# Kernel tuning notes

Hardware: AMD Instinct MI355X
Metric: run time of the kernel (lower is better)

Reference implementation:

```python
import jax, jax.numpy as jnp
import numpy as np

B, N, SU, H, NC, NUM_ITER = 1024, 32, 8, 64, 4, 5
E = N * (N - 1)


def _edge_idx(n):
    # Fully-connected graph without self loops; edges grouped contiguously by
    # destination node so that blocks of (n-1) messages sum into one node
    # (matches the original Python segment-sum loop with step = n-1).
    idx = np.arange(n)
    temp_a = np.concatenate([np.delete(idx, j) for j in range(n)])  # sources
    temp_b = np.repeat(idx, n - 1)                                   # destinations
    return temp_a, temp_b


def _lin(x, W, b):
    return x @ W.T + b


def setup_inputs():
    key = jax.random.key(0)
    ks = jax.random.split(key, 20)
    f = jax.random.normal
    return {
        "read_gru": f(ks[0], (B, N, SU), jnp.float32),
        "gru_init": f(ks[1], (B, N, H), jnp.float32),
        "init_features": f(ks[2], (B, N, 3), jnp.float32),
        "edge_weight": f(ks[3], (B, E), jnp.float32),
        "noise_info": jax.random.uniform(ks[4], (B, 1), jnp.float32),
        "x_hat_EP": f(ks[5], (B, N), jnp.float32),
        "variance_EP": jax.random.uniform(ks[6], (B, N), jnp.float32),
        "W1a": f(ks[7], (SU, 3)) * 0.3, "b1a": jnp.zeros((SU,)),
        "W2a": f(ks[8], (H, 2 * SU + 2)) * 0.1, "b2a": jnp.zeros((H,)),
        "W2b": f(ks[9], (H // 2, H)) * 0.1, "b2b": jnp.zeros((H // 2,)),
        "W2c": f(ks[10], (SU, H // 2)) * 0.1, "b2c": jnp.zeros((SU,)),
        "Wih": f(ks[11], (3 * H, SU + 2)) * 0.1, "bih": jnp.zeros((3 * H,)),
        "Whh": f(ks[12], (3 * H, H)) * 0.1, "bhh": jnp.zeros((3 * H,)),
        "W3a": f(ks[13], (H, SU)) * 0.1, "b3a": jnp.zeros((H,)),
        "W3b": f(ks[14], (H // 2, H)) * 0.1, "b3b": jnp.zeros((H // 2,)),
        "W3c": f(ks[15], (NC, H // 2)) * 0.1, "b3c": jnp.zeros((NC,)),
        "W4": f(ks[16], (SU, H)) * 0.1, "b4": jnp.zeros((SU,)),
        "GNN_iter": 0,
    }


def reference(read_gru, gru_init, init_features, edge_weight, noise_info,
              x_hat_EP, variance_EP,
              W1a, b1a, W2a, b2a, W2b, b2b, W2c, b2c,
              Wih, bih, Whh, bhh,
              W3a, b3a, W3b, b3b, W3c, b3c, W4, b4, GNN_iter):
    b, n = init_features.shape[0], init_features.shape[1]
    temp_a, temp_b = _edge_idx(n)
    e = temp_a.shape[0]
    edge_e = edge_weight[:, :, None]                              # [B,E,1]
    noise_e = jnp.broadcast_to(noise_info, (b, e))[:, :, None]    # [B,E,1]
    gru_hidden = gru_init
    for it in range(NUM_ITER):
        if it == 0 and GNN_iter == 0:
            init_nodes = _lin(init_features, W1a, b1a)            # [B,N,SU]
        else:
            init_nodes = read_gru
        s1 = init_nodes[:, temp_a, :]                             # gather sources
        s2 = init_nodes[:, temp_b, :]                             # gather dests
        comb = jnp.concatenate([s1, s2, edge_e, noise_e], axis=2) # [B,E,2SU+2]
        m = jax.nn.relu(_lin(comb, W2a, b2a))
        m = jax.nn.relu(_lin(m, W2b, b2b))
        m = jax.nn.relu(_lin(m, W2c, b2c))                        # [B,E,SU]
        # contiguous blocks of (n-1) messages per destination node
        sum_msgs = m.reshape(b, n, n - 1, -1).sum(axis=2)         # [B,N,SU]
        gin = jnp.concatenate(
            [sum_msgs, x_hat_EP[:, :, None], variance_EP[:, :, None]], axis=2)
        # GRUCell applied per node
        gi = _lin(gin, Wih, bih)
        gh = _lin(gru_hidden, Whh, bhh)
        i_r, i_z, i_n = jnp.split(gi, 3, axis=-1)
        h_r, h_z, h_n = jnp.split(gh, 3, axis=-1)
        r = jax.nn.sigmoid(i_r + h_r)
        z = jax.nn.sigmoid(i_z + h_z)
        cand = jnp.tanh(i_n + r * h_n)
        gru_hidden = (1.0 - z) * cand + z * gru_hidden
        read_gru = _lin(gru_hidden, W4, b4)
    # readout (no activations in original forward)
    p_y_x = _lin(_lin(_lin(read_gru, W3a, b3a), W3b, b3b), W3c, b3c)
    return (p_y_x, read_gru, gru_hidden)
```

## Files before the change

kernel.cpp:

```cpp
#include <hip/hip_runtime.h>
#include <hip/hip_bf16.h>

#define BB 1024
#define NN 32
#define SUD 8
#define HD 64
#define NCD 4
#define ED 992
#define NITER 5

#define O_W2AT 0
#define O_B2A  1152
#define O_W2B  1216
#define O_B2B  3264
#define O_W2CT 3296
#define O_B2C  3552
#define O_WIHT 3560
#define O_BIH  5480
#define O_WHHT 5672
#define O_BHH  17960
#define O_W4T  18152
#define O_B4   18664
#define O_W3AT 18672
#define O_B3A  19184
#define O_W3BT 19248
#define O_B3B  21296
#define O_W3CT 21328
#define O_B3C  21456
#define O_W1AT 21460
#define O_B1A  21484
#define W_TOTAL 21492
#define O_WIHP 21492
#define W_TOTAL2 25332

#define FRAG_B2   0
#define FRAG_C    2048
#define FRAG_WHH  2560
#define FRAG_A2P  14848
#define FRAG_TOTAL 18944
#define PREP_TOTAL (W_TOTAL2 + FRAG_TOTAL)

typedef const float* fwp;
typedef __attribute__((ext_vector_type(8))) short short8;
typedef __attribute__((ext_vector_type(4))) float float4v;
typedef __attribute__((ext_vector_type(2))) float float2v;

__device__ __forceinline__ short bf16r(float x) {
  __hip_bfloat16 h = __float2bfloat16(x);
  return __builtin_bit_cast(short, h);
}

__global__ void prep_weights(fwp W2a, fwp b2a, fwp W2b, fwp b2b, fwp W2c, fwp b2c,
                             fwp Wih, fwp bih, fwp Whh, fwp bhh,
                             fwp W3a, fwp b3a, fwp W3b, fwp b3b, fwp W3c, fwp b3c,
                             fwp W4, fwp b4, fwp W1a, fwp b1a, float* __restrict__ ws) {
  int idx = blockIdx.x * 256 + threadIdx.x;
  if (idx >= PREP_TOTAL) return;
  if (idx >= W_TOTAL2) {
    __hip_bfloat16* wbw = (__hip_bfloat16*)(ws + W_TOTAL2);
    int e = idx - W_TOTAL2;
    float v;
    if (e < 2048) {
      int j = e & 7, L = (e >> 3) & 63, hs = e >> 9;
      int h = hs >> 1, s = hs & 1;
      v = W2b[(2 * (L & 15) + h) * 64 + s * 32 + ((L >> 4) & 3) * 8 + j];
    } else if (e < 2560) {
      int e2 = e - 2048;
      int j = e2 & 7, L = (e2 >> 3) & 63;
      int su = L & 15, q = L >> 4;
      v = (su < 8) ? W2c[su * 32 + q * 8 + j] : 0.f;
    } else if (e < 14848) {
      int e2 = e - 2560;
      int j = e2 & 7, L = (e2 >> 3) & 63, nts = e2 >> 9;
      int nt = nts >> 1, s = nts & 1;
      v = Whh[(nt * 16 + (L & 15)) * 64 + s * 32 + ((L >> 4) & 3) * 8 + j];
    } else {
      int e2 = e - 14848;
      int j = e2 & 7, L = (e2 >> 3) & 63, nt = e2 >> 9;
      int col = L & 15, kq = L >> 4;
      v = 0.f;
      if (kq == 0) v = (nt < 4) ? W2a[(nt * 16 + col) * 18 + j]
                                : W2a[((nt - 4) * 16 + col) * 18 + 8 + j];
    }
    wbw[e] = __float2bfloat16(v);
    return;
  }
  if (idx >= W_TOTAL) {
    int p = idx - O_WIHP;
    int o = p / 20, k = (p % 20) >> 1;
    ws[idx] = Wih[o * 10 + k];
    return;
  }
  float v;
  if (idx < O_B2A)       { int p = idx;          int su = p / 64, f = p % 64;   v = W2a[f * 18 + su]; }
  else if (idx < O_W2B)  { v = b2a[idx - O_B2A]; }
  else if (idx < O_B2B)  { v = W2b[idx - O_W2B]; }
  else if (idx < O_W2CT) { v = b2b[idx - O_B2B]; }
  else if (idx < O_B2C)  { int p = idx - O_W2CT; int o = p / 8, su = p % 8;     v = W2c[su * 32 + o]; }
  else if (idx < O_WIHT) { v = b2c[idx - O_B2C]; }
  else if (idx < O_BIH)  { int p = idx - O_WIHT; int k = p / 192, o = p % 192;  v = Wih[o * 10 + k]; }
  else if (idx < O_WHHT) { v = bih[idx - O_BIH]; }
  else if (idx < O_BHH)  {
    int p = idx - O_WHHT;
    if (p < 3072) {
      unsigned packed = 0;
#pragma unroll
      for (int h = 0; h < 2; ++h) {
        int e = 2 * p + h;
        int j = e & 7, L = (e >> 3) & 63, nt = e >> 9;
        int k = ((L >> 4) & 3) * 8 + j;
        float vv = (k < 10) ? Wih[(nt * 16 + (L & 15)) * 10 + k] : 0.f;
        unsigned us = (unsigned short)bf16r(vv);
        packed |= us << (16 * h);
      }
      ws[idx] = __builtin_bit_cast(float, packed);
      return;
    }
    int k = p / 192, o = p % 192;  v = Whh[o * 64 + k];
  }
  else if (idx < O_W4T)  { v = bhh[idx - O_BHH]; }
  else if (idx < O_B4)   { int p = idx - O_W4T;  int k = p / 8, su = p % 8;     v = W4[su * 64 + k]; }
  else if (idx < O_W3AT) { v = b4[idx - O_B4]; }
  else if (idx < O_B3A)  { int p = idx - O_W3AT; int k = p / 64, f = p % 64;    v = W3a[f * 8 + k]; }
  else if (idx < O_W3BT) { v = b3a[idx - O_B3A]; }
  else if (idx < O_B3B)  { int p = idx - O_W3BT; int k = p / 32, f = p % 32;    v = W3b[f * 64 + k]; }
  else if (idx < O_W3CT) { v = b3b[idx - O_B3B]; }
  else if (idx < O_B3C)  { int p = idx - O_W3CT; int k = p / 4, c = p % 4;      v = W3c[c * 32 + k]; }
  else if (idx < O_W1AT) { v = b3c[idx - O_B3C]; }
  else if (idx < O_B1A)  { int p = idx - O_W1AT; int c = p / 8, su = p % 8;     v = W1a[su * 3 + c]; }
  else                   { v = b1a[idx - O_B1A]; }
  ws[idx] = v;
}

#define DO_STEP2(AROW, EWV, KOFF, Y0, Y1, W0, W1, FH0, FH1, ACC0, ACC1)        \
  {                                                                            \
    float4v x0 = *(const float4v*)&sA1[(AROW) * 68 + (KOFF)];                  \
    float4v x1 = *(const float4v*)&sA1[(AROW) * 68 + (KOFF) + 4];              \
    float4v z4 = {0.f, 0.f, 0.f, 0.f};                                         \
    float4v t0 = (x0 + Y0) + (EWV) * W0;                                       \
    float4v t1 = (x1 + Y1) + (EWV) * W1;                                       \
    t0 = __builtin_elementwise_max(t0, z4);                                    \
    t1 = __builtin_elementwise_max(t1, z4);                                    \
    short8 ahi;                                                                \
    ahi[0] = bf16r(t0.x); ahi[1] = bf16r(t0.y); ahi[2] = bf16r(t0.z);          \
    ahi[3] = bf16r(t0.w); ahi[4] = bf16r(t1.x); ahi[5] = bf16r(t1.y);          \
    ahi[6] = bf16r(t1.z); ahi[7] = bf16r(t1.w);                                \
    ACC0 = __builtin_amdgcn_mfma_f32_16x16x32_bf16(ahi, FH0, ACC0, 0, 0, 0);   \
    ACC1 = __builtin_amdgcn_mfma_f32_16x16x32_bf16(ahi, FH1, ACC1, 0, 0, 0);   \
  }

#define LAUNDER(v) __asm__ __volatile__("" : "+v"(v))

__global__ __launch_bounds__(256, 4) void gnn_fused(
    const float* __restrict__ read_gru_in,
    const float* __restrict__ gru_init,
    const float* __restrict__ feat,
    const float* __restrict__ edge_w,
    const float* __restrict__ noise_in,
    const float* __restrict__ xhat,
    const float* __restrict__ vep,
    const int* __restrict__ gnn_iter_p,
    const float* __restrict__ ws,
    const float* __restrict__ W4g,
    float* __restrict__ out)
{
  __shared__ __attribute__((aligned(16))) char spool[23040];
  __shared__ __attribute__((aligned(16))) float sH[NN * 68];
  __shared__ float sNodes[NN * 9];
  __shared__ float sSum[NN * 8];
  __shared__ float sEw[ED];
  __shared__ float sC1[64];
  __shared__ float sWew[64];
  __shared__ float sX[NN];
  __shared__ float sV[NN];

  float* const sA1 = (float*)spool;
  float* const sA2 = (float*)(spool + 8704);
  __hip_bfloat16* const sM2 = (__hip_bfloat16*)(spool + 17408);

  const int b = blockIdx.x;
  const int t = threadIdx.x;
  const int lane = t & 63;
  const int wv = t >> 6;
  const int quad = lane >> 4;
  const int lm = lane & 15;

  const __hip_bfloat16* wb = (const __hip_bfloat16*)(ws + W_TOTAL2);

  float noi = noise_in[b];
  for (int e = t; e < ED; e += 256) sEw[e] = edge_w[b * ED + e];
  if (t < NN) { sX[t] = xhat[b * NN + t]; sV[t] = vep[b * NN + t]; }
  if (t < 64) {
    sC1[t]  = ws[O_B2A + t] + noi * ws[O_W2AT + 17 * 64 + t];
    sWew[t] = ws[O_W2AT + 16 * 64 + t];
  }
#pragma unroll
  for (int i = 0; i < 8; ++i) {
    int p = t + 256 * i;
    sH[(p >> 6) * 68 + (p & 63)] = gru_init[b * (NN * HD) + p];
  }
  {
    const int git = gnn_iter_p[0];
    int n = t >> 3, su = t & 7;
    float acc;
    if (git == 0) {
      acc = ws[O_B1A + su];
#pragma unroll
      for (int c = 0; c < 3; ++c)
        acc += ws[O_W1AT + c * 8 + su] * feat[b * (NN * 3) + n * 3 + c];
    } else {
      acc = read_gru_in[b * (NN * SUD) + t];
    }
    sNodes[n * 9 + su] = acc;
  }
  __syncthreads();

  for (int it = 0; it < NITER; ++it) {
    int ive = 0; LAUNDER(ive);
    const float* wsle = ws + ive;
    const __hip_bfloat16* wble = wb + ive;
    short8 fbh00 = *(const short8*)(wble + FRAG_B2 + (0 * 64 + lane) * 8);
    short8 fbh01 = *(const short8*)(wble + FRAG_B2 + (1 * 64 + lane) * 8);
    short8 fbh10 = *(const short8*)(wble + FRAG_B2 + (2 * 64 + lane) * 8);
    short8 fbh11 = *(const short8*)(wble + FRAG_B2 + (3 * 64 + lane) * 8);
    short8 fcf   = *(const short8*)(wble + FRAG_C + lane * 8);
    const float2v b2bv = *(const float2v*)&wsle[O_B2B + 2 * lm];
    const float   b2cl = wsle[O_B2C + lm];

    {
      int iva = 0; LAUNDER(iva);
      const __hip_bfloat16* fp = wb + FRAG_A2P + iva;
      short8 aN[2];
#pragma unroll
      for (int mt = 0; mt < 2; ++mt) {
        short8 a = {0, 0, 0, 0, 0, 0, 0, 0};
        if (quad == 0) {
          const float* np = &sNodes[(mt * 16 + lm) * 9];
#pragma unroll
          for (int q = 0; q < 8; ++q) a[q] = bf16r(np[q]);
        }
        aN[mt] = a;
      }
      const int f = wv * 16 + lm;
      const float c1f = sC1[f];
#pragma unroll
      for (int half = 0; half < 2; ++half) {
        short8 bfr = *(const short8*)(fp + ((half * 4 + wv) * 64 + lane) * 8);
#pragma unroll
        for (int mt = 0; mt < 2; ++mt) {
          float4v acc = {0.f, 0.f, 0.f, 0.f};
          acc = __builtin_amdgcn_mfma_f32_16x16x32_bf16(aN[mt], bfr, acc, 0, 0, 0);
#pragma unroll
          for (int r = 0; r < 4; ++r) {
            int node = mt * 16 + quad * 4 + r;
            if (half == 0) sA1[node * 68 + f] = acc[r];
            else           sA2[node * 68 + f] = acc[r] + c1f;
          }
        }
      }
    }
    __syncthreads();

    {
      int ivz = 0; LAUNDER(ivz);
      __hip_bfloat16* m2w = sM2 + wv * (16 * 44);
      const int kq0 = quad * 8, kq1 = 32 + quad * 8;
      float4v wwA = *(const float4v*)&sWew[ivz + kq0];
      float4v wwB = *(const float4v*)&sWew[ivz + kq0 + 4];
      float4v wwC = *(const float4v*)&sWew[ivz + kq1];
      float4v wwD = *(const float4v*)&sWew[ivz + kq1 + 4];
      const float4v binit0 = {b2bv.x, b2bv.x, b2bv.x, b2bv.x};
      const float4v binit1 = {b2bv.y, b2bv.y, b2bv.y, b2bv.y};
      const float4v cinit  = {b2cl, b2cl, b2cl, b2cl};
      const int kkB = 16 + lm;
      const int kkB2 = (kkB < 31) ? kkB : 0;
      for (int ni = 0; ni < 8; ++ni) {
        const int jj = wv * 8 + ni;
        const int a0 = lm + (lm >= jj ? 1 : 0);
        const int a1 = kkB2 + (kkB2 >= jj ? 1 : 0);
        const float ew0 = sEw[ivz + jj * 31 + lm];
        const float ew1 = (kkB < 31) ? sEw[ivz + jj * 31 + kkB] : 0.f;
        float4v yA = *(const float4v*)&sA2[jj * 68 + kq0];
        float4v yB = *(const float4v*)&sA2[jj * 68 + kq0 + 4];
        float4v yC = *(const float4v*)&sA2[jj * 68 + kq1];
        float4v yD = *(const float4v*)&sA2[jj * 68 + kq1 + 4];
        float4v acc00 = binit0;
        float4v acc01 = binit1;
        DO_STEP2(a0, ew0, kq0, yA, yB, wwA, wwB, fbh00, fbh10, acc00, acc01);
        DO_STEP2(a0, ew0, kq1, yC, yD, wwC, wwD, fbh01, fbh11, acc00, acc01);
#pragma unroll
        for (int r = 0; r < 4; ++r) {
          float m20 = fmaxf(acc00[r], 0.f);
          float m21 = fmaxf(acc01[r], 0.f);
          ushort2 pp;
          pp.x = (unsigned short)bf16r(m20);
          pp.y = (unsigned short)bf16r(m21);
          *(ushort2*)(m2w + (quad * 4 + r) * 44 + 2 * lm) = pp;
        }
        float4v acc10 = binit0;
        float4v acc11 = binit1;
        DO_STEP2(a1, ew1, kq0, yA, yB, wwA, wwB, fbh00, fbh10, acc10, acc11);
        DO_STEP2(a1, ew1, kq1, yC, yD, wwC, wwD, fbh01, fbh11, acc10, acc11);
        __asm__ __volatile__("" ::: "memory");
        float psum;
        {
          short8 ac = *(const short8*)(m2w + lm * 44 + quad * 8);
          float4v c3 = cinit;
          c3 = __builtin_amdgcn_mfma_f32_16x16x32_bf16(ac, fcf, c3, 0, 0, 0);
          psum  = fmaxf(c3[0], 0.f);
          psum += fmaxf(c3[1], 0.f);
          psum += fmaxf(c3[2], 0.f);
          psum += fmaxf(c3[3], 0.f);
        }
        __asm__ __volatile__("" ::: "memory");
#pragma unroll
        for (int r = 0; r < 4; ++r) {
          float m20 = fmaxf(acc10[r], 0.f);
          float m21 = fmaxf(acc11[r], 0.f);
          ushort2 pp;
          pp.x = (unsigned short)bf16r(m20);
          pp.y = (unsigned short)bf16r(m21);
          *(ushort2*)(m2w + (quad * 4 + r) * 44 + 2 * lm) = pp;
        }
        __asm__ __volatile__("" ::: "memory");
        {
          short8 ac = *(const short8*)(m2w + lm * 44 + quad * 8);
          float4v c3 = cinit;
          c3 = __builtin_amdgcn_mfma_f32_16x16x32_bf16(ac, fcf, c3, 0, 0, 0);
#pragma unroll
          for (int r = 0; r < 4; ++r) {
            float v = fmaxf(c3[r], 0.f);
            if (r == 3) v = (quad == 3) ? 0.f : v;
            psum += v;
          }
        }
        __asm__ __volatile__("" ::: "memory");
        psum += __shfl_xor(psum, 16);
        psum += __shfl_xor(psum, 32);
        if (lane < 8) sSum[jj * 8 + lane] = psum;
      }
    }
    __syncthreads();

    {
      int ivg = 0; LAUNDER(ivg);
      const __hip_bfloat16* wbl = wb + ivg;
      const __hip_bfloat16* wihf = (const __hip_bfloat16*)(ws + O_WHHT) + ivg;
      short8 aH[2][2];
      short8 aG[2];
#pragma unroll
      for (int mt = 0; mt < 2; ++mt) {
#pragma unroll
        for (int s = 0; s < 2; ++s) {
          const float* hp = &sH[(mt * 16 + lm) * 68 + s * 32 + quad * 8];
          float4v h0 = *(const float4v*)hp;
          float4v h1 = *(const float4v*)(hp + 4);
          short8 a;
          a[0] = bf16r(h0.x); a[1] = bf16r(h0.y); a[2] = bf16r(h0.z); a[3] = bf16r(h0.w);
          a[4] = bf16r(h1.x); a[5] = bf16r(h1.y); a[6] = bf16r(h1.z); a[7] = bf16r(h1.w);
          aH[mt][s] = a;
        }
        short8 g = {0, 0, 0, 0, 0, 0, 0, 0};
        int nrow = mt * 16 + lm;
        if (quad == 0) {
          float4v s0 = *(const float4v*)&sSum[nrow * 8];
          float4v s1 = *(const float4v*)&sSum[nrow * 8 + 4];
          g[0] = bf16r(s0.x); g[1] = bf16r(s0.y); g[2] = bf16r(s0.z); g[3] = bf16r(s0.w);
          g[4] = bf16r(s1.x); g[5] = bf16r(s1.y); g[6] = bf16r(s1.z); g[7] = bf16r(s1.w);
        } else if (quad == 1) {
          g[0] = bf16r(sX[nrow]);
          g[1] = bf16r(sV[nrow]);
        }
        aG[mt] = g;
      }
      const float4v zz4 = {0.f, 0.f, 0.f, 0.f};
      float4v pr0, pr1, pz0, pz1, phn0, phn1, pin0, pin1;
      {
        int gnt = wv;
        short8 bh0 = *(const short8*)(wbl + FRAG_WHH + ((gnt * 2 + 0) * 64 + lane) * 8);
        short8 bh1 = *(const short8*)(wbl + FRAG_WHH + ((gnt * 2 + 1) * 64 + lane) * 8);
        short8 bwi = *(const short8*)(wihf + (gnt * 64 + lane) * 8);
        pr0 = __builtin_amdgcn_mfma_f32_16x16x32_bf16(aG[0], bwi, zz4, 0, 0, 0);
        pr0 = __builtin_amdgcn_mfma_f32_16x16x32_bf16(aH[0][0], bh0, pr0, 0, 0, 0);
        pr0 = __builtin_amdgcn_mfma_f32_16x16x32_bf16(aH[0][1], bh1, pr0, 0, 0, 0);
        pr1 = __builtin_amdgcn_mfma_f32_16x16x32_bf16(aG[1], bwi, zz4, 0, 0, 0);
        pr1 = __builtin_amdgcn_mfma_f32_16x16x32_bf16(aH[1][0], bh0, pr1, 0, 0, 0);
        pr1 = __builtin_amdgcn_mfma_f32_16x16x32_bf16(aH[1][1], bh1, pr1, 0, 0, 0);
      }
      {
        int gnt = 4 + wv;
        short8 bh0 = *(const short8*)(wbl + FRAG_WHH + ((gnt * 2 + 0) * 64 + lane) * 8);
        short8 bh1 = *(const short8*)(wbl + FRAG_WHH + ((gnt * 2 + 1) * 64 + lane) * 8);
        short8 bwi = *(const short8*)(wihf + (gnt * 64 + lane) * 8);
        pz0 = __builtin_amdgcn_mfma_f32_16x16x32_bf16(aG[0], bwi, zz4, 0, 0, 0);
        pz0 = __builtin_amdgcn_mfma_f32_16x16x32_bf16(aH[0][0], bh0, pz0, 0, 0, 0);
        pz0 = __builtin_amdgcn_mfma_f32_16x16x32_bf16(aH[0][1], bh1, pz0, 0, 0, 0);
        pz1 = __builtin_amdgcn_mfma_f32_16x16x32_bf16(aG[1], bwi, zz4, 0, 0, 0);
        pz1 = __builtin_amdgcn_mfma_f32_16x16x32_bf16(aH[1][0], bh0, pz1, 0, 0, 0);
        pz1 = __builtin_amdgcn_mfma_f32_16x16x32_bf16(aH[1][1], bh1, pz1, 0, 0, 0);
      }
      {
        int gnt = 8 + wv;
        short8 bh0 = *(const short8*)(wbl + FRAG_WHH + ((gnt * 2 + 0) * 64 + lane) * 8);
        short8 bh1 = *(const short8*)(wbl + FRAG_WHH + ((gnt * 2 + 1) * 64 + lane) * 8);
        short8 bwi = *(const short8*)(wihf + (gnt * 64 + lane) * 8);
        phn0 = __builtin_amdgcn_mfma_f32_16x16x32_bf16(aH[0][0], bh0, zz4, 0, 0, 0);
        phn0 = __builtin_amdgcn_mfma_f32_16x16x32_bf16(aH[0][1], bh1, phn0, 0, 0, 0);
        phn1 = __builtin_amdgcn_mfma_f32_16x16x32_bf16(aH[1][0], bh0, zz4, 0, 0, 0);
        phn1 = __builtin_amdgcn_mfma_f32_16x16x32_bf16(aH[1][1], bh1, phn1, 0, 0, 0);
        pin0 = __builtin_amdgcn_mfma_f32_16x16x32_bf16(aG[0], bwi, zz4, 0, 0, 0);
        pin1 = __builtin_amdgcn_mfma_f32_16x16x32_bf16(aG[1], bwi, zz4, 0, 0, 0);
      }
      const int c = wv * 16 + lm;
      const float br  = ws[O_BIH + c]       + ws[O_BHH + c];
      const float bz  = ws[O_BIH + 64 + c]  + ws[O_BHH + 64 + c];
      const float bni = ws[O_BIH + 128 + c];
      const float bnh = ws[O_BHH + 128 + c];
      float4v hn0, hn1;
#pragma unroll
      for (int mt = 0; mt < 2; ++mt) {
#pragma unroll
        for (int rr = 0; rr < 4; ++rr) {
          int n = mt * 16 + quad * 4 + rr;
          float pre_r = ((mt == 0) ? pr0[rr]  : pr1[rr])  + br;
          float pre_z = ((mt == 0) ? pz0[rr]  : pz1[rr])  + bz;
          float i_n   = ((mt == 0) ? pin0[rr] : pin1[rr]) + bni;
          float h_n   = ((mt == 0) ? phn0[rr] : phn1[rr]) + bnh;
          float er = __expf(-pre_r);
          float r = __builtin_amdgcn_rcpf(1.f + er);
          float ez = __expf(-pre_z);
          float z = __builtin_amdgcn_rcpf(1.f + ez);
          float cd = i_n + r * h_n;
          float e2 = __expf(2.f * cd);
          float th = 1.f - 2.f * __builtin_amdgcn_rcpf(e2 + 1.f);
          float hv = sH[n * 68 + c];
          float hnew = th + z * (hv - th);
          if (mt == 0) hn0[rr] = hnew; else hn1[rr] = hnew;
        }
      }
      __syncthreads();
#pragma unroll
      for (int rr = 0; rr < 4; ++rr) {
        sH[(quad * 4 + rr) * 68 + c]      = hn0[rr];
        sH[(16 + quad * 4 + rr) * 68 + c] = hn1[rr];
      }
    }
    __syncthreads();

    {
      int ivw = 0; LAUNDER(ivw);
      int n = t >> 3, su = t & 7;
      const float* w4r = W4g + ivw + su * 64;
      float4v acc4 = {0.f, 0.f, 0.f, 0.f};
#pragma unroll
      for (int k = 0; k < 64; k += 4) {
        float4v w = *(const float4v*)&w4r[k];
        float4v h = *(const float4v*)&sH[n * 68 + k];
        acc4 += w * h;
      }
      sNodes[n * 9 + su] = ws[O_B4 + su] + ((acc4.x + acc4.y) + (acc4.z + acc4.w));
    }
    __syncthreads();
  }

#pragma unroll
  for (int i = 0; i < 8; ++i) {
    int p = t + 256 * i;
    int n = p >> 6, f = p & 63;
    float acc = ws[O_B3A + f];
#pragma unroll
    for (int k = 0; k < 8; ++k) acc += ws[O_W3AT + k * 64 + f] * sNodes[n * 9 + k];
    sA1[n * 68 + f] = acc;
  }
  __syncthreads();
#pragma unroll
  for (int i = 0; i < 4; ++i) {
    int p = t + 256 * i;
    int n = p >> 5, f = p & 31;
    float c0 = 0.f, c1v = 0.f, c2 = 0.f, c3v = 0.f;
#pragma unroll
    for (int k = 0; k < 64; k += 4) {
      c0  += ws[O_W3BT + (k + 0) * 32 + f] * sA1[n * 68 + k + 0];
      c1v += ws[O_W3BT + (k + 1) * 32 + f] * sA1[n * 68 + k + 1];
      c2  += ws[O_W3BT + (k + 2) * 32 + f] * sA1[n * 68 + k + 2];
      c3v += ws[O_W3BT + (k + 3) * 32 + f] * sA1[n * 68 + k + 3];
    }
    sA2[n * 33 + f] = ws[O_B3B + f] + ((c0 + c1v) + (c2 + c3v));
  }
  __syncthreads();
  if (t < 128) {
    int n = t >> 2, c = t & 3;
    float acc = ws[O_B3C + c];
#pragma unroll
    for (int k = 0; k < 32; ++k) acc += ws[O_W3CT + k * 4 + c] * sA2[n * 33 + k];
    out[b * (NN * NCD) + t] = acc;
  }
  out[BB * NN * NCD + b * (NN * SUD) + t] = sNodes[(t >> 3) * 9 + (t & 7)];
#pragma unroll
  for (int i = 0; i < 8; ++i) {
    int p = t + 256 * i;
    out[BB * NN * NCD + BB * NN * SUD + b * (NN * HD) + p] =
        sH[(p >> 6) * 68 + (p & 63)];
  }
}

extern "C" void kernel_launch(void* const* d_in, const int* in_sizes, int n_in,
                              void* d_out, int out_size, void* d_ws, size_t ws_size,
                              hipStream_t stream) {
  typedef const float* F32;
  F32 read_gru = (F32)d_in[0];
  F32 gru_init = (F32)d_in[1];
  F32 feat     = (F32)d_in[2];
  F32 edge_w   = (F32)d_in[3];
  F32 noise    = (F32)d_in[4];
  F32 xh       = (F32)d_in[5];
  F32 vp       = (F32)d_in[6];
  F32 W1a = (F32)d_in[7];  F32 b1a = (F32)d_in[8];
  F32 W2a = (F32)d_in[9];  F32 b2a = (F32)d_in[10];
  F32 W2b = (F32)d_in[11]; F32 b2b = (F32)d_in[12];
  F32 W2c = (F32)d_in[13]; F32 b2c = (F32)d_in[14];
  F32 Wih = (F32)d_in[15]; F32 bih = (F32)d_in[16];
  F32 Whh = (F32)d_in[17]; F32 bhh = (F32)d_in[18];
  F32 W3a = (F32)d_in[19]; F32 b3a = (F32)d_in[20];
  F32 W3b = (F32)d_in[21]; F32 b3b = (F32)d_in[22];
  F32 W3c = (F32)d_in[23]; F32 b3c = (F32)d_in[24];
  F32 W4  = (F32)d_in[25]; F32 b4  = (F32)d_in[26];
  const int* git = (const int*)d_in[27];
  float* ws = (float*)d_ws;

  prep_weights<<<(PREP_TOTAL + 255) / 256, 256, 0, stream>>>(
      W2a, b2a, W2b, b2b, W2c, b2c, Wih, bih, Whh, bhh,
      W3a, b3a, W3b, b3b, W3c, b3c, W4, b4, W1a, b1a, ws);

  gnn_fused<<<BB, 256, 0, stream>>>(read_gru, gru_init, feat, edge_w, noise,
                                    xh, vp, git, ws, W4, (float*)d_out);
}
```

Baseline: 245.5 us.

## Fold W4 readout into first message layer weights for later iterations

Precomputes the products W2a·W4 (for both source and destination halves) and b4·W2a at weight-prep time, so iterations after the first compute the first message-layer pre-activations directly from the GRU hidden state with K=64 MFMAs. This removes the per-iteration W4 projection and its barrier, moving it to a single computation after the loop. In exchange it reuses the W2B/W2CT/WIHP workspace slots for the folded weights and runs four MFMAs per tile instead of one, and rounds the folded weights and hidden state to bf16.

```diff
diff --git a/kernel.cpp b/kernel.cpp
--- a/kernel.cpp
+++ b/kernel.cpp
@@ -87,16 +87,58 @@
   }
   if (idx >= W_TOTAL) {
     int p = idx - O_WIHP;
-    int o = p / 20, k = (p % 20) >> 1;
-    ws[idx] = Wih[o * 10 + k];
+    if (p < 2048) {
+      unsigned packed = 0;
+#pragma unroll
+      for (int h = 0; h < 2; ++h) {
+        int e = 2 * p + h;
+        int j = e & 7, L = (e >> 3) & 63, fts = e >> 9;
+        int ft = fts >> 1, s = fts & 1;
+        int f = ft * 16 + (L & 15);
+        int k = s * 32 + ((L >> 4) & 3) * 8 + j;
+        float acc = 0.f;
+        for (int su = 0; su < 8; ++su) acc += W2a[f * 18 + 8 + su] * W4[su * 64 + k];
+        unsigned us = (unsigned short)bf16r(acc);
+        packed |= us << (16 * h);
+      }
+      ws[idx] = __builtin_bit_cast(float, packed);
+    } else {
+      ws[idx] = 0.f;
+    }
     return;
   }
   float v;
   if (idx < O_B2A)       { int p = idx;          int su = p / 64, f = p % 64;   v = W2a[f * 18 + su]; }
   else if (idx < O_W2B)  { v = b2a[idx - O_B2A]; }
-  else if (idx < O_B2B)  { v = W2b[idx - O_W2B]; }
+  else if (idx < O_B2B)  {
+    int p = idx - O_W2B;
+    unsigned packed = 0;
+#pragma unroll
+    for (int h = 0; h < 2; ++h) {
+      int e = 2 * p + h;
+      int j = e & 7, L = (e >> 3) & 63, fts = e >> 9;
+      int ft = fts >> 1, s = fts & 1;
+      int f = ft * 16 + (L & 15);
+      int k = s * 32 + ((L >> 4) & 3) * 8 + j;
+      float acc = 0.f;
+      for (int su = 0; su < 8; ++su) acc += W2a[f * 18 + su] * W4[su * 64 + k];
+      unsigned us = (unsigned short)bf16r(acc);
+      packed |= us << (16 * h);
+    }
+    ws[idx] = __builtin_bit_cast(float, packed);
+    return;
+  }
   else if (idx < O_W2CT) { v = b2b[idx - O_B2B]; }
-  else if (idx < O_B2C)  { int p = idx - O_W2CT; int o = p / 8, su = p % 8;     v = W2c[su * 32 + o]; }
+  else if (idx < O_B2C)  {
+    int p = idx - O_W2CT;
+    float acc = 0.f;
+    if (p < 128) {
+      int f = p & 63;
+      int off = (p < 64) ? 0 : 8;
+      for (int su = 0; su < 8; ++su) acc += b4[su] * W2a[f * 18 + off + su];
+    }
+    v = acc;
+  }
   else if (idx < O_WIHT) { v = b2c[idx - O_B2C]; }
   else if (idx < O_BIH)  { int p = idx - O_WIHT; int k = p / 192, o = p % 192;  v = Wih[o * 10 + k]; }
   else if (idx < O_WHHT) { v = bih[idx - O_BIH]; }
@@ -227,7 +269,7 @@
     const float2v b2bv = *(const float2v*)&wsle[O_B2B + 2 * lm];
     const float   b2cl = wsle[O_B2C + lm];
 
-    {
+    if (it == 0) {
       int iva = 0; LAUNDER(iva);
       const __hip_bfloat16* fp = wb + FRAG_A2P + iva;
       short8 aN[2];
@@ -256,6 +298,46 @@
             if (half == 0) sA1[node * 68 + f] = acc[r];
             else           sA2[node * 68 + f] = acc[r] + c1f;
           }
+        }
+      }
+    } else {
+      int iva = 0; LAUNDER(iva);
+      const __hip_bfloat16* wc1 = (const __hip_bfloat16*)(ws + O_W2B) + iva;
+      const __hip_bfloat16* wc2 = (const __hip_bfloat16*)(ws + O_WIHP) + iva;
+      short8 aH2[2][2];
+#pragma unroll
+      for (int mt = 0; mt < 2; ++mt) {
+#pragma unroll
+        for (int s = 0; s < 2; ++s) {
+          const float* hp = &sH[(mt * 16 + lm) * 68 + s * 32 + quad * 8];
+          float4v h0 = *(const float4v*)hp;
+          float4v h1 = *(const float4v*)(hp + 4);
+          short8 a;
+          a[0] = bf16r(h0.x); a[1] = bf16r(h0.y); a[2] = bf16r(h0.z); a[3] = bf16r(h0.w);
+          a[4] = bf16r(h1.x); a[5] = bf16r(h1.y); a[6] = bf16r(h1.z); a[7] = bf16r(h1.w);
+          aH2[mt][s] = a;
+        }
+      }
+      const int f = wv * 16 + lm;
+      const float cb1f = ws[O_W2CT + f];
+      const float cb2f = ws[O_W2CT + 64 + f] + sC1[f];
+      short8 w10 = *(const short8*)(wc1 + ((wv * 2 + 0) * 64 + lane) * 8);
+      short8 w11 = *(const short8*)(wc1 + ((wv * 2 + 1) * 64 + lane) * 8);
+      short8 w20 = *(const short8*)(wc2 + ((wv * 2 + 0) * 64 + lane) * 8);
+      short8 w21 = *(const short8*)(wc2 + ((wv * 2 + 1) * 64 + lane) * 8);
+#pragma unroll
+      for (int mt = 0; mt < 2; ++mt) {
+        float4v a1 = {cb1f, cb1f, cb1f, cb1f};
+        a1 = __builtin_amdgcn_mfma_f32_16x16x32_bf16(aH2[mt][0], w10, a1, 0, 0, 0);
+        a1 = __builtin_amdgcn_mfma_f32_16x16x32_bf16(aH2[mt][1], w11, a1, 0, 0, 0);
+        float4v a2 = {cb2f, cb2f, cb2f, cb2f};
+        a2 = __builtin_amdgcn_mfma_f32_16x16x32_bf16(aH2[mt][0], w20, a2, 0, 0, 0);
+        a2 = __builtin_amdgcn_mfma_f32_16x16x32_bf16(aH2[mt][1], w21, a2, 0, 0, 0);
+#pragma unroll
+        for (int r = 0; r < 4; ++r) {
+          int node = mt * 16 + quad * 4 + r;
+          sA1[node * 68 + f] = a1[r];
+          sA2[node * 68 + f] = a2[r];
         }
       }
     }
@@ -446,22 +528,22 @@
       }
     }
     __syncthreads();
-
-    {
-      int ivw = 0; LAUNDER(ivw);
-      int n = t >> 3, su = t & 7;
-      const float* w4r = W4g + ivw + su * 64;
-      float4v acc4 = {0.f, 0.f, 0.f, 0.f};
-#pragma unroll
-      for (int k = 0; k < 64; k += 4) {
-        float4v w = *(const float4v*)&w4r[k];
-        float4v h = *(const float4v*)&sH[n * 68 + k];
-        acc4 += w * h;
-      }
-      sNodes[n * 9 + su] = ws[O_B4 + su] + ((acc4.x + acc4.y) + (acc4.z + acc4.w));
-    }
-    __syncthreads();
-  }
+  }
+
+  {
+    int ivw = 0; LAUNDER(ivw);
+    int n = t >> 3, su = t & 7;
+    const float* w4r = W4g + ivw + su * 64;
+    float4v acc4 = {0.f, 0.f, 0.f, 0.f};
+#pragma unroll
+    for (int k = 0; k < 64; k += 4) {
+      float4v w = *(const float4v*)&w4r[k];
+      float4v h = *(const float4v*)&sH[n * 68 + k];
+      acc4 += w * h;
+    }
+    sNodes[n * 9 + su] = ws[O_B4 + su] + ((acc4.x + acc4.y) + (acc4.z + acc4.w));
+  }
+  __syncthreads();
 
 #pragma unroll
   for (int i = 0; i < 8; ++i) {
```

Result: slower. 257.3 us (+4.8%).
